# Kernel optimization log

Hardware: AMD Instinct MI355X
Metric: run time of the kernel (lower is better)

The kernel has to match this reference:

```python
import jax, jax.numpy as jnp
import numpy as np

B, C, H, W = 16, 256, 32, 32
NUM_LAYERS = 30
OUT = 16  # sqrt(out_channels)
EPS = 1e-5


def setup_inputs() -> dict:
    key = jax.random.key(0)
    k1, k2, k3 = jax.random.split(key, 3)
    x = jax.random.normal(k1, (B, C, H, W), dtype=jnp.float32)
    # delta_t ~ small positive values (module inits ~N(0.01, 0.005))
    delta_t = jax.random.uniform(k2, (NUM_LAYERS, 1), dtype=jnp.float32) * 0.02
    matrices = jax.random.normal(k3, (NUM_LAYERS, 1, 1, OUT, OUT), dtype=jnp.float32) * 0.1
    gamma = jnp.ones((H * W,), dtype=jnp.float32)   # BatchNorm2d weight, oc = i*i = H*W
    beta = jnp.zeros((H * W,), dtype=jnp.float32)   # BatchNorm2d bias
    return {"x": x, "delta_t": delta_t, "matrices": matrices, "gamma": gamma, "beta": beta}


def _bn_relu6(z, gamma, beta):
    # training-mode BatchNorm2d over channel axis 1 (channels = H*W), then ReLU6
    mean = jnp.mean(z, axis=(0, 2, 3), keepdims=True)
    var = jnp.mean(jnp.square(z - mean), axis=(0, 2, 3), keepdims=True)  # biased var
    zhat = (z - mean) * jax.lax.rsqrt(var + EPS)
    g = gamma.reshape(1, -1, 1, 1)
    b = beta.reshape(1, -1, 1, 1)
    return jnp.clip(zhat * g + b, 0.0, 6.0)


def reference(x, delta_t, matrices, gamma, beta):
    b, c, h, w = x.shape
    hw = h * w
    # feature_reshape: [B,C,H,W] -> [B,HW,C] -> [B,HW,out,out] (inn == out branch)
    x1 = x.reshape(b, c, hw).transpose(0, 2, 1).reshape(b, hw, OUT, OUT)
    dt = jnp.clip(delta_t, 0.0, 6.0)[:, 0]  # relu6(delta_t), shape [L]

    def step(y0, params):
        m, dtl = params  # m: [1,1,out,out] broadcasts elementwise against x1
        dydt = -y0 + _bn_relu6(y0 + m * x1, gamma, beta)
        return y0 + dtl * dydt, None

    y0, _ = jax.lax.scan(step, x1, (matrices, dt))
    # (y0 + x1): [B, HW, out, out] -> view [B,H,W,out*out] -> permute to [B,out*out,H,W]
    y = (y0 + x1).reshape(b, h, w, OUT * OUT).transpose(0, 3, 1, 2)
    return y
```

## Files before the change

### kernel.cpp

```cpp
#include <hip/hip_runtime.h>

typedef float v2f __attribute__((ext_vector_type(2)));
typedef float v4f __attribute__((ext_vector_type(4)));

#define HW      1024
#define NROWS   4096
#define NLAYERS 30
#define TPB     256

static __device__ __forceinline__ v2f pk_fma(v2f a, v2f b, v2f c) {
    v2f d; asm("v_pk_fma_f32 %0, %1, %2, %3" : "=v"(d) : "v"(a), "v"(b), "v"(c));
    return d;
}
static __device__ __forceinline__ v2f pk_add(v2f a, v2f b) {
    v2f d; asm("v_pk_add_f32 %0, %1, %2" : "=v"(d) : "v"(a), "v"(b));
    return d;
}
static __device__ __forceinline__ v2f pk_mul(v2f a, v2f b) {
    v2f d; asm("v_pk_mul_f32 %0, %1, %2" : "=v"(d) : "v"(a), "v"(b));
    return d;
}

template <int CTRL, int RMASK>
__device__ __forceinline__ float dpp_add(float x) {
    int t = __builtin_amdgcn_update_dpp(0, __builtin_bit_cast(int, x),
                                        CTRL, RMASK, 0xf, true);
    return x + __builtin_bit_cast(float, t);
}
__device__ __forceinline__ float wave_sum64(float x) {
    x = dpp_add<0x111, 0xf>(x);
    x = dpp_add<0x112, 0xf>(x);
    x = dpp_add<0x114, 0xf>(x);
    x = dpp_add<0x118, 0xf>(x);
    x = dpp_add<0x142, 0xa>(x);
    x = dpp_add<0x143, 0xc>(x);
    return x;
}
__device__ __forceinline__ float bcast63(float x) {
    return __builtin_bit_cast(float,
        __builtin_amdgcn_readlane(__builtin_bit_cast(int, x), 63));
}

__global__ __launch_bounds__(TPB) void txp64(const float* __restrict__ src,
                                             float* __restrict__ dst,
                                             int M, int N) {
    __shared__ float tile[64][65];
    const int n0 = blockIdx.x * 64;
    const int m0 = blockIdx.y * 64;
    const int tx = threadIdx.x & 63;
    const int ty = threadIdx.x >> 6;
#pragma unroll
    for (int i = 0; i < 16; ++i) {
        const int r = ty + 4 * i;
        tile[r][tx] = src[(size_t)(m0 + r) * N + n0 + tx];
    }
    __syncthreads();
#pragma unroll
    for (int i = 0; i < 16; ++i) {
        const int r = ty + 4 * i;
        dst[(size_t)(n0 + r) * M + m0 + tx] = tile[tx][r];
    }
}

__global__ __launch_bounds__(64, 1) void ode_row1w(
    float* ws, const float* __restrict__ delta_t,
    const float* __restrict__ matrices, const float* __restrict__ gamma,
    const float* __restrict__ beta) {

    const int p    = blockIdx.x;
    const int lane = threadIdx.x;
    float* row = ws + (size_t)p * NROWS;

    v2f x1[32], y[32], z[32];
#pragma unroll
    for (int j = 0; j < 16; ++j) {
        const v4f q4 = *(const v4f*)(row + 4 * lane + 256 * j);
        x1[2 * j]     = (v2f){q4.x, q4.y};
        x1[2 * j + 1] = (v2f){q4.z, q4.w};
        y[2 * j]     = x1[2 * j];
        y[2 * j + 1] = x1[2 * j + 1];
    }

    const float gp = gamma[p];
    const float bp = beta[p];

    v2f sa[4], qa[4];

    {
        const v4f m4 = *(const v4f*)(matrices + 4 * lane);
        const v2f mA = {m4.x, m4.y}, mB = {m4.z, m4.w};
#pragma unroll
        for (int r = 0; r < 4; ++r) { sa[r] = (v2f){0.f, 0.f}; qa[r] = (v2f){0.f, 0.f}; }
#pragma unroll
        for (int j = 0; j < 16; ++j) {
            z[2 * j]     = pk_fma(mA, x1[2 * j], y[2 * j]);
            z[2 * j + 1] = pk_fma(mB, x1[2 * j + 1], y[2 * j + 1]);
            sa[j & 3] = pk_add(sa[j & 3], z[2 * j]);
            qa[j & 3] = pk_fma(z[2 * j], z[2 * j], qa[j & 3]);
            sa[(j + 2) & 3] = pk_add(sa[(j + 2) & 3], z[2 * j + 1]);
            qa[(j + 2) & 3] = pk_fma(z[2 * j + 1], z[2 * j + 1], qa[(j + 2) & 3]);
        }
    }

    v4f   mq  = *(const v4f*)(matrices + 256 + 4 * lane);
    float dtc = delta_t[0];
    float dtn = delta_t[1];

    for (int k = 0; k < NLAYERS - 1; ++k) {
        const int k2 = (k + 2 < NLAYERS) ? k + 2 : NLAYERS - 1;
        const v4f   mq_n  = *(const v4f*)(matrices + k2 * 256 + 4 * lane);
        const float dt_nn = delta_t[k2];

        const v2f sv = pk_add(pk_add(sa[0], sa[1]), pk_add(sa[2], sa[3]));
        const v2f qv = pk_add(pk_add(qa[0], qa[1]), pk_add(qa[2], qa[3]));
        const float S = bcast63(wave_sum64(sv.x + sv.y));
        const float Q = bcast63(wave_sum64(qv.x + qv.y));

        const float dtk  = __builtin_amdgcn_fmed3f(dtc, 0.0f, 6.0f);
        const float mean = S * (1.0f / 4096.0f);
        const float var  = fmaf(-mean, mean, Q * (1.0f / 4096.0f));
        const float rstd = rsqrtf(var + 1e-5f);
        const float g    = gp * rstd;
        const float b    = fmaf(-mean, g, bp);
        const v2f g2 = {g, g}, b2 = {b, b};
        const v2f dt2 = {dtk, dtk};
        const v2f om2 = {1.0f - dtk, 1.0f - dtk};
        const v2f mA = {mq.x, mq.y}, mB = {mq.z, mq.w};

#pragma unroll
        for (int r = 0; r < 4; ++r) { sa[r] = (v2f){0.f, 0.f}; qa[r] = (v2f){0.f, 0.f}; }

#pragma unroll
        for (int j = 0; j < 16; ++j) {
#pragma unroll
            for (int h = 0; h < 2; ++h) {
                const int e = 2 * j + h;
                v2f a = pk_fma(z[e], g2, b2);
                a.x = __builtin_amdgcn_fmed3f(a.x, 0.0f, 6.0f);
                a.y = __builtin_amdgcn_fmed3f(a.y, 0.0f, 6.0f);
                v2f yy = pk_mul(om2, y[e]);
                y[e] = pk_fma(dt2, a, yy);
                z[e] = pk_fma(h ? mB : mA, x1[e], y[e]);
                sa[(j + 2 * h) & 3] = pk_add(sa[(j + 2 * h) & 3], z[e]);
                qa[(j + 2 * h) & 3] = pk_fma(z[e], z[e], qa[(j + 2 * h) & 3]);
            }
        }

        mq = mq_n; dtc = dtn; dtn = dt_nn;
    }

    {
        const v2f sv = pk_add(pk_add(sa[0], sa[1]), pk_add(sa[2], sa[3]));
        const v2f qv = pk_add(pk_add(qa[0], qa[1]), pk_add(qa[2], qa[3]));
        const float S = bcast63(wave_sum64(sv.x + sv.y));
        const float Q = bcast63(wave_sum64(qv.x + qv.y));

        const float dtk  = __builtin_amdgcn_fmed3f(dtc, 0.0f, 6.0f);
        const float mean = S * (1.0f / 4096.0f);
        const float var  = fmaf(-mean, mean, Q * (1.0f / 4096.0f));
        const float rstd = rsqrtf(var + 1e-5f);
        const float g    = gp * rstd;
        const float b    = fmaf(-mean, g, bp);
        const v2f g2 = {g, g}, b2 = {b, b};
        const v2f dt2 = {dtk, dtk};
        const v2f om2 = {1.0f - dtk, 1.0f - dtk};

#pragma unroll
        for (int j = 0; j < 16; ++j) {
            v2f o0, o1;
#pragma unroll
            for (int h = 0; h < 2; ++h) {
                const int e = 2 * j + h;
                v2f a = pk_fma(z[e], g2, b2);
                a.x = __builtin_amdgcn_fmed3f(a.x, 0.0f, 6.0f);
                a.y = __builtin_amdgcn_fmed3f(a.y, 0.0f, 6.0f);
                v2f yy = pk_mul(om2, y[e]);
                yy = pk_fma(dt2, a, yy);
                const v2f o = pk_add(yy, x1[e]);
                if (h == 0) o0 = o; else o1 = o;
            }
            v4f o4; o4.x = o0.x; o4.y = o0.y; o4.z = o1.x; o4.w = o1.y;
            *(v4f*)(row + 4 * lane + 256 * j) = o4;
        }
    }
}

__global__ __launch_bounds__(TPB) void ode_fused(const float* __restrict__ x,
                                                 const float* __restrict__ delta_t,
                                                 const float* __restrict__ matrices,
                                                 const float* __restrict__ gamma,
                                                 const float* __restrict__ beta,
                                                 float* __restrict__ out) {
    const int bid = blockIdx.x;
    const int p   = ((bid & 7) << 7) | (bid >> 3);
    const int t   = threadIdx.x;

    __shared__ float smat[(NLAYERS + 1) * 256];
    __shared__ float sdt[NLAYERS];
    __shared__ __align__(16) v2f red[2][4];

#pragma unroll
    for (int i = 0; i < NLAYERS; ++i)
        smat[i * 256 + t] = matrices[i * 256 + t];
    if (t < NLAYERS)
        sdt[t] = __builtin_amdgcn_fmed3f(delta_t[t], 0.0f, 6.0f);

    v2f x1[8], y[8];
#pragma unroll
    for (int k = 0; k < 8; ++k) {
        x1[k].x = x[(size_t)(t + 512 * k) * HW + p];
        x1[k].y = x[(size_t)(t + 512 * k + 256) * HW + p];
        y[k] = x1[k];
    }

    const float gp   = gamma[p];
    const float bp   = beta[p];
    const int   wid  = t >> 6;
    const int   lane = t & 63;

    __syncthreads();
    float m_cur = smat[t];

    for (int l = 0; l < NLAYERS; ++l) {
        const float dtl = sdt[l];
        const v2f m2    = {m_cur, m_cur};
        const v2f dt2   = {dtl, dtl};
        const v2f om2   = {1.0f - dtl, 1.0f - dtl};

        v2f z[8];
        v2f sA = {0.f, 0.f}, sB = {0.f, 0.f};
        v2f qA = {0.f, 0.f}, qB = {0.f, 0.f};
#pragma unroll
        for (int k = 0; k < 8; k += 2) {
            z[k]     = __builtin_elementwise_fma(m2, x1[k], y[k]);
            z[k + 1] = __builtin_elementwise_fma(m2, x1[k + 1], y[k + 1]);
            sA += z[k];
            sB += z[k + 1];
            qA = __builtin_elementwise_fma(z[k], z[k], qA);
            qB = __builtin_elementwise_fma(z[k + 1], z[k + 1], qB);
        }
#pragma unroll
        for (int k = 0; k < 8; ++k) y[k] *= om2;

        const v2f sv = sA + sB;
        const v2f qv = qA + qB;
        float s = wave_sum64(sv.x + sv.y);
        float q = wave_sum64(qv.x + qv.y);

        const int par = l & 1;
        if (lane == 63) { v2f w; w.x = s; w.y = q; red[par][wid] = w; }
        m_cur = smat[(l + 1) * 256 + t];
        __syncthreads();

        const float4 r0 = *(const float4*)&red[par][0];
        const float4 r1 = *(const float4*)&red[par][2];
        const float S  = (r0.x + r0.z) + (r1.x + r1.z);
        const float S2 = (r0.y + r0.w) + (r1.y + r1.w);

        const float mean = S * (1.0f / 4096.0f);
        const float var  = fmaf(-mean, mean, S2 * (1.0f / 4096.0f));
        const float rstd = rsqrtf(var + 1e-5f);
        const float g    = gp * rstd;
        const float bb   = fmaf(-mean, g, bp);
        const v2f g2 = {g, g}, b2 = {bb, bb};
        const v2f z0 = {0.f, 0.f}, s6 = {6.f, 6.f};
#pragma unroll
        for (int k = 0; k < 8; ++k) {
            v2f a = __builtin_elementwise_fma(z[k], g2, b2);
            a = __builtin_elementwise_max(a, z0);
            a = __builtin_elementwise_min(a, s6);
            y[k] = __builtin_elementwise_fma(dt2, a, y[k]);
        }
    }

#pragma unroll
    for (int k = 0; k < 8; ++k) {
        out[(size_t)(t + 512 * k) * HW + p]       = y[k].x + x1[k].x;
        out[(size_t)(t + 512 * k + 256) * HW + p] = y[k].y + x1[k].y;
    }
}

extern "C" void kernel_launch(void* const* d_in, const int* in_sizes, int n_in,
                              void* d_out, int out_size, void* d_ws, size_t ws_size,
                              hipStream_t stream) {
    const float* x        = (const float*)d_in[0];
    const float* delta_t  = (const float*)d_in[1];
    const float* matrices = (const float*)d_in[2];
    const float* gamma    = (const float*)d_in[3];
    const float* beta     = (const float*)d_in[4];
    float* out = (float*)d_out;

    const size_t need = (size_t)HW * NROWS * sizeof(float);
    if (d_ws != nullptr && ws_size >= need) {
        float* ws = (float*)d_ws;
        txp64<<<dim3(HW / 64, NROWS / 64), dim3(TPB), 0, stream>>>(x, ws, NROWS, HW);
        ode_row1w<<<dim3(HW), dim3(64), 0, stream>>>(ws, delta_t, matrices, gamma, beta);
        txp64<<<dim3(NROWS / 64, HW / 64), dim3(TPB), 0, stream>>>(ws, out, HW, NROWS);
    } else {
        ode_fused<<<dim3(HW), dim3(TPB), 0, stream>>>(x, delta_t, matrices, gamma, beta, out);
    }
}
```

Before: 111.7 us.

## Split each BN channel row across two waves with LDS double-buffered reduction

The per-channel ODE kernel now uses two 64-lane waves per row instead of one, so each lane holds 16 packed pairs instead of 32. Per-layer mean/variance partials are combined through a double-buffered shared-memory slot with one barrier per layer. The aim is to halve per-wave serial work and register pressure, raising wave count and latency hiding across 1024 blocks. In exchange, each of the 30 layers now pays a block barrier and an LDS round trip.

```diff
diff --git a/kernel.cpp b/kernel.cpp
--- a/kernel.cpp
+++ b/kernel.cpp
@@ -36,10 +36,6 @@
     x = dpp_add<0x143, 0xc>(x);
     return x;
 }
-__device__ __forceinline__ float bcast63(float x) {
-    return __builtin_bit_cast(float,
-        __builtin_amdgcn_readlane(__builtin_bit_cast(int, x), 63));
-}
 
 __global__ __launch_bounds__(TPB) void txp64(const float* __restrict__ src,
                                              float* __restrict__ dst,
@@ -62,19 +58,24 @@
     }
 }
 
-__global__ __launch_bounds__(64, 1) void ode_row1w(
+__global__ __launch_bounds__(128, 2) void ode_row2w(
     float* ws, const float* __restrict__ delta_t,
     const float* __restrict__ matrices, const float* __restrict__ gamma,
     const float* __restrict__ beta) {
 
     const int p    = blockIdx.x;
-    const int lane = threadIdx.x;
+    const int t    = threadIdx.x;
+    const int wid  = t >> 6;
+    const int lane = t & 63;
+    const int c0   = (4 * t) & 255;
     float* row = ws + (size_t)p * NROWS;
 
-    v2f x1[32], y[32], z[32];
-#pragma unroll
-    for (int j = 0; j < 16; ++j) {
-        const v4f q4 = *(const v4f*)(row + 4 * lane + 256 * j);
+    __shared__ __align__(16) v2f red[2][2];
+
+    v2f x1[16], y[16], z[16];
+#pragma unroll
+    for (int j = 0; j < 8; ++j) {
+        const v4f q4 = *(const v4f*)(row + 4 * t + 512 * j);
         x1[2 * j]     = (v2f){q4.x, q4.y};
         x1[2 * j + 1] = (v2f){q4.z, q4.w};
         y[2 * j]     = x1[2 * j];
@@ -84,37 +85,40 @@
     const float gp = gamma[p];
     const float bp = beta[p];
 
-    v2f sa[4], qa[4];
-
     {
-        const v4f m4 = *(const v4f*)(matrices + 4 * lane);
+        const v4f m4 = *(const v4f*)(matrices + c0);
         const v2f mA = {m4.x, m4.y}, mB = {m4.z, m4.w};
-#pragma unroll
-        for (int r = 0; r < 4; ++r) { sa[r] = (v2f){0.f, 0.f}; qa[r] = (v2f){0.f, 0.f}; }
-#pragma unroll
-        for (int j = 0; j < 16; ++j) {
+        v2f s0 = {0.f, 0.f}, s1 = {0.f, 0.f}, q0 = {0.f, 0.f}, q1 = {0.f, 0.f};
+#pragma unroll
+        for (int j = 0; j < 8; ++j) {
             z[2 * j]     = pk_fma(mA, x1[2 * j], y[2 * j]);
             z[2 * j + 1] = pk_fma(mB, x1[2 * j + 1], y[2 * j + 1]);
-            sa[j & 3] = pk_add(sa[j & 3], z[2 * j]);
-            qa[j & 3] = pk_fma(z[2 * j], z[2 * j], qa[j & 3]);
-            sa[(j + 2) & 3] = pk_add(sa[(j + 2) & 3], z[2 * j + 1]);
-            qa[(j + 2) & 3] = pk_fma(z[2 * j + 1], z[2 * j + 1], qa[(j + 2) & 3]);
-        }
-    }
-
-    v4f   mq  = *(const v4f*)(matrices + 256 + 4 * lane);
+            s0 = pk_add(s0, z[2 * j]);
+            q0 = pk_fma(z[2 * j], z[2 * j], q0);
+            s1 = pk_add(s1, z[2 * j + 1]);
+            q1 = pk_fma(z[2 * j + 1], z[2 * j + 1], q1);
+        }
+        const v2f sv = pk_add(s0, s1);
+        const v2f qv = pk_add(q0, q1);
+        const float ss = wave_sum64(sv.x + sv.y);
+        const float qq = wave_sum64(qv.x + qv.y);
+        if (lane == 63) red[0][wid] = (v2f){ss, qq};
+    }
+
+    v4f   mq  = *(const v4f*)(matrices + 256 + c0);
     float dtc = delta_t[0];
     float dtn = delta_t[1];
+    __syncthreads();
 
     for (int k = 0; k < NLAYERS - 1; ++k) {
         const int k2 = (k + 2 < NLAYERS) ? k + 2 : NLAYERS - 1;
-        const v4f   mq_n  = *(const v4f*)(matrices + k2 * 256 + 4 * lane);
+        const v4f   mq_n  = *(const v4f*)(matrices + k2 * 256 + c0);
         const float dt_nn = delta_t[k2];
 
-        const v2f sv = pk_add(pk_add(sa[0], sa[1]), pk_add(sa[2], sa[3]));
-        const v2f qv = pk_add(pk_add(qa[0], qa[1]), pk_add(qa[2], qa[3]));
-        const float S = bcast63(wave_sum64(sv.x + sv.y));
-        const float Q = bcast63(wave_sum64(qv.x + qv.y));
+        const int par = k & 1;
+        const v4f r = *(const v4f*)&red[par][0];
+        const float S = r.x + r.z;
+        const float Q = r.y + r.w;
 
         const float dtk  = __builtin_amdgcn_fmed3f(dtc, 0.0f, 6.0f);
         const float mean = S * (1.0f / 4096.0f);
@@ -127,11 +131,9 @@
         const v2f om2 = {1.0f - dtk, 1.0f - dtk};
         const v2f mA = {mq.x, mq.y}, mB = {mq.z, mq.w};
 
-#pragma unroll
-        for (int r = 0; r < 4; ++r) { sa[r] = (v2f){0.f, 0.f}; qa[r] = (v2f){0.f, 0.f}; }
-
-#pragma unroll
-        for (int j = 0; j < 16; ++j) {
+        v2f s0 = {0.f, 0.f}, s1 = {0.f, 0.f}, q0 = {0.f, 0.f}, q1 = {0.f, 0.f};
+#pragma unroll
+        for (int j = 0; j < 8; ++j) {
 #pragma unroll
             for (int h = 0; h < 2; ++h) {
                 const int e = 2 * j + h;
@@ -141,19 +143,24 @@
                 v2f yy = pk_mul(om2, y[e]);
                 y[e] = pk_fma(dt2, a, yy);
                 z[e] = pk_fma(h ? mB : mA, x1[e], y[e]);
-                sa[(j + 2 * h) & 3] = pk_add(sa[(j + 2 * h) & 3], z[e]);
-                qa[(j + 2 * h) & 3] = pk_fma(z[e], z[e], qa[(j + 2 * h) & 3]);
+                if (h == 0) { s0 = pk_add(s0, z[e]); q0 = pk_fma(z[e], z[e], q0); }
+                else        { s1 = pk_add(s1, z[e]); q1 = pk_fma(z[e], z[e], q1); }
             }
         }
+        const v2f sv = pk_add(s0, s1);
+        const v2f qv = pk_add(q0, q1);
+        const float ss = wave_sum64(sv.x + sv.y);
+        const float qq = wave_sum64(qv.x + qv.y);
+        if (lane == 63) red[par ^ 1][wid] = (v2f){ss, qq};
 
         mq = mq_n; dtc = dtn; dtn = dt_nn;
+        __syncthreads();
     }
 
     {
-        const v2f sv = pk_add(pk_add(sa[0], sa[1]), pk_add(sa[2], sa[3]));
-        const v2f qv = pk_add(pk_add(qa[0], qa[1]), pk_add(qa[2], qa[3]));
-        const float S = bcast63(wave_sum64(sv.x + sv.y));
-        const float Q = bcast63(wave_sum64(qv.x + qv.y));
+        const v4f r = *(const v4f*)&red[(NLAYERS - 1) & 1][0];
+        const float S = r.x + r.z;
+        const float Q = r.y + r.w;
 
         const float dtk  = __builtin_amdgcn_fmed3f(dtc, 0.0f, 6.0f);
         const float mean = S * (1.0f / 4096.0f);
@@ -166,7 +173,7 @@
         const v2f om2 = {1.0f - dtk, 1.0f - dtk};
 
 #pragma unroll
-        for (int j = 0; j < 16; ++j) {
+        for (int j = 0; j < 8; ++j) {
             v2f o0, o1;
 #pragma unroll
             for (int h = 0; h < 2; ++h) {
@@ -180,7 +187,7 @@
                 if (h == 0) o0 = o; else o1 = o;
             }
             v4f o4; o4.x = o0.x; o4.y = o0.y; o4.z = o1.x; o4.w = o1.y;
-            *(v4f*)(row + 4 * lane + 256 * j) = o4;
+            *(v4f*)(row + 4 * t + 512 * j) = o4;
         }
     }
 }
@@ -294,7 +301,7 @@
     if (d_ws != nullptr && ws_size >= need) {
         float* ws = (float*)d_ws;
         txp64<<<dim3(HW / 64, NROWS / 64), dim3(TPB), 0, stream>>>(x, ws, NROWS, HW);
-        ode_row1w<<<dim3(HW), dim3(64), 0, stream>>>(ws, delta_t, matrices, gamma, beta);
+        ode_row2w<<<dim3(HW), dim3(128), 0, stream>>>(ws, delta_t, matrices, gamma, beta);
         txp64<<<dim3(NROWS / 64, HW / 64), dim3(TPB), 0, stream>>>(ws, out, HW, NROWS);
     } else {
         ode_fused<<<dim3(HW), dim3(TPB), 0, stream>>>(x, delta_t, matrices, gamma, beta, out);
```

New measurement: 115.3 us. 1.03x slower.

## Track pre-activation z recurrence and keep x1 in LDS to cut registers

Applied to the files above, without the earlier changes.

Rewrites the ODE step to update z = y + m*x1 directly using a combined coefficient (m_next - (1-dt)*m_cur), removing the y register array. The x1 values are stored in shared memory and reloaded each layer instead of living in registers. This reduces VGPR pressure, which may allow more waves per CU, at the cost of LDS reads every layer and shorter reduction accumulator chains.

```diff
diff --git a/kernel.cpp b/kernel.cpp
--- a/kernel.cpp
+++ b/kernel.cpp
@@ -62,57 +62,53 @@
     }
 }
 
-__global__ __launch_bounds__(64, 1) void ode_row1w(
+__global__ __launch_bounds__(64, 1) void ode_zrec(
     float* ws, const float* __restrict__ delta_t,
     const float* __restrict__ matrices, const float* __restrict__ gamma,
     const float* __restrict__ beta) {
 
     const int p    = blockIdx.x;
     const int lane = threadIdx.x;
+    const int c0   = 4 * lane;
     float* row = ws + (size_t)p * NROWS;
 
-    v2f x1[32], y[32], z[32];
-#pragma unroll
-    for (int j = 0; j < 16; ++j) {
-        const v4f q4 = *(const v4f*)(row + 4 * lane + 256 * j);
-        x1[2 * j]     = (v2f){q4.x, q4.y};
-        x1[2 * j + 1] = (v2f){q4.z, q4.w};
-        y[2 * j]     = x1[2 * j];
-        y[2 * j + 1] = x1[2 * j + 1];
-    }
+    __shared__ float xs[NROWS];
 
     const float gp = gamma[p];
     const float bp = beta[p];
 
-    v2f sa[4], qa[4];
+    v2f z[32];
+    v2f s0 = {0.f, 0.f}, s1 = {0.f, 0.f}, q0 = {0.f, 0.f}, q1 = {0.f, 0.f};
 
     {
-        const v4f m4 = *(const v4f*)(matrices + 4 * lane);
+        const v4f m4 = *(const v4f*)(matrices + c0);
         const v2f mA = {m4.x, m4.y}, mB = {m4.z, m4.w};
 #pragma unroll
-        for (int r = 0; r < 4; ++r) { sa[r] = (v2f){0.f, 0.f}; qa[r] = (v2f){0.f, 0.f}; }
-#pragma unroll
         for (int j = 0; j < 16; ++j) {
-            z[2 * j]     = pk_fma(mA, x1[2 * j], y[2 * j]);
-            z[2 * j + 1] = pk_fma(mB, x1[2 * j + 1], y[2 * j + 1]);
-            sa[j & 3] = pk_add(sa[j & 3], z[2 * j]);
-            qa[j & 3] = pk_fma(z[2 * j], z[2 * j], qa[j & 3]);
-            sa[(j + 2) & 3] = pk_add(sa[(j + 2) & 3], z[2 * j + 1]);
-            qa[(j + 2) & 3] = pk_fma(z[2 * j + 1], z[2 * j + 1], qa[(j + 2) & 3]);
-        }
-    }
-
-    v4f   mq  = *(const v4f*)(matrices + 256 + 4 * lane);
+            const v4f x4 = *(const v4f*)(row + 4 * lane + 256 * j);
+            *(v4f*)&xs[4 * lane + 256 * j] = x4;
+            const v2f xA = {x4.x, x4.y}, xB = {x4.z, x4.w};
+            z[2 * j]     = pk_fma(mA, xA, xA);
+            z[2 * j + 1] = pk_fma(mB, xB, xB);
+            s0 = pk_add(s0, z[2 * j]);
+            q0 = pk_fma(z[2 * j], z[2 * j], q0);
+            s1 = pk_add(s1, z[2 * j + 1]);
+            q1 = pk_fma(z[2 * j + 1], z[2 * j + 1], q1);
+        }
+    }
+
+    v4f   mqc = *(const v4f*)(matrices + c0);
+    v4f   mqn = *(const v4f*)(matrices + 256 + c0);
     float dtc = delta_t[0];
     float dtn = delta_t[1];
 
     for (int k = 0; k < NLAYERS - 1; ++k) {
         const int k2 = (k + 2 < NLAYERS) ? k + 2 : NLAYERS - 1;
-        const v4f   mq_n  = *(const v4f*)(matrices + k2 * 256 + 4 * lane);
+        const v4f   mq2   = *(const v4f*)(matrices + k2 * 256 + c0);
         const float dt_nn = delta_t[k2];
 
-        const v2f sv = pk_add(pk_add(sa[0], sa[1]), pk_add(sa[2], sa[3]));
-        const v2f qv = pk_add(pk_add(qa[0], qa[1]), pk_add(qa[2], qa[3]));
+        const v2f sv = pk_add(s0, s1);
+        const v2f qv = pk_add(q0, q1);
         const float S = bcast63(wave_sum64(sv.x + sv.y));
         const float Q = bcast63(wave_sum64(qv.x + qv.y));
 
@@ -122,36 +118,53 @@
         const float rstd = rsqrtf(var + 1e-5f);
         const float g    = gp * rstd;
         const float b    = fmaf(-mean, g, bp);
+        const float om   = 1.0f - dtk;
         const v2f g2 = {g, g}, b2 = {b, b};
         const v2f dt2 = {dtk, dtk};
-        const v2f om2 = {1.0f - dtk, 1.0f - dtk};
-        const v2f mA = {mq.x, mq.y}, mB = {mq.z, mq.w};
-
-#pragma unroll
-        for (int r = 0; r < 4; ++r) { sa[r] = (v2f){0.f, 0.f}; qa[r] = (v2f){0.f, 0.f}; }
+        const v2f om2 = {om, om};
+        const v2f omn = {-om, -om};
+        const v2f mcA = {mqc.x, mqc.y}, mcB = {mqc.z, mqc.w};
+        const v2f mnA = {mqn.x, mqn.y}, mnB = {mqn.z, mqn.w};
+        const v2f dmA = pk_fma(omn, mcA, mnA);
+        const v2f dmB = pk_fma(omn, mcB, mnB);
+
+        s0 = (v2f){0.f, 0.f}; s1 = (v2f){0.f, 0.f};
+        q0 = (v2f){0.f, 0.f}; q1 = (v2f){0.f, 0.f};
 
 #pragma unroll
         for (int j = 0; j < 16; ++j) {
-#pragma unroll
-            for (int h = 0; h < 2; ++h) {
-                const int e = 2 * j + h;
+            const v4f x4 = *(const v4f*)&xs[4 * lane + 256 * j];
+            const v2f xA = {x4.x, x4.y}, xB = {x4.z, x4.w};
+            {
+                const int e = 2 * j;
                 v2f a = pk_fma(z[e], g2, b2);
                 a.x = __builtin_amdgcn_fmed3f(a.x, 0.0f, 6.0f);
                 a.y = __builtin_amdgcn_fmed3f(a.y, 0.0f, 6.0f);
-                v2f yy = pk_mul(om2, y[e]);
-                y[e] = pk_fma(dt2, a, yy);
-                z[e] = pk_fma(h ? mB : mA, x1[e], y[e]);
-                sa[(j + 2 * h) & 3] = pk_add(sa[(j + 2 * h) & 3], z[e]);
-                qa[(j + 2 * h) & 3] = pk_fma(z[e], z[e], qa[(j + 2 * h) & 3]);
+                v2f t = pk_mul(dt2, a);
+                t = pk_fma(dmA, xA, t);
+                z[e] = pk_fma(om2, z[e], t);
+                s0 = pk_add(s0, z[e]);
+                q0 = pk_fma(z[e], z[e], q0);
             }
-        }
-
-        mq = mq_n; dtc = dtn; dtn = dt_nn;
+            {
+                const int e = 2 * j + 1;
+                v2f a = pk_fma(z[e], g2, b2);
+                a.x = __builtin_amdgcn_fmed3f(a.x, 0.0f, 6.0f);
+                a.y = __builtin_amdgcn_fmed3f(a.y, 0.0f, 6.0f);
+                v2f t = pk_mul(dt2, a);
+                t = pk_fma(dmB, xB, t);
+                z[e] = pk_fma(om2, z[e], t);
+                s1 = pk_add(s1, z[e]);
+                q1 = pk_fma(z[e], z[e], q1);
+            }
+        }
+
+        mqc = mqn; mqn = mq2; dtc = dtn; dtn = dt_nn;
     }
 
     {
-        const v2f sv = pk_add(pk_add(sa[0], sa[1]), pk_add(sa[2], sa[3]));
-        const v2f qv = pk_add(pk_add(qa[0], qa[1]), pk_add(qa[2], qa[3]));
+        const v2f sv = pk_add(s0, s1);
+        const v2f qv = pk_add(q0, q1);
         const float S = bcast63(wave_sum64(sv.x + sv.y));
         const float Q = bcast63(wave_sum64(qv.x + qv.y));
 
@@ -161,23 +174,38 @@
         const float rstd = rsqrtf(var + 1e-5f);
         const float g    = gp * rstd;
         const float b    = fmaf(-mean, g, bp);
+        const float om   = 1.0f - dtk;
         const v2f g2 = {g, g}, b2 = {b, b};
         const v2f dt2 = {dtk, dtk};
-        const v2f om2 = {1.0f - dtk, 1.0f - dtk};
+        const v2f om2 = {om, om};
+        const v2f omn = {-om, -om};
+        const v2f one2 = {1.0f, 1.0f};
+        const v2f mcA = {mqc.x, mqc.y}, mcB = {mqc.z, mqc.w};
+        const v2f dmA = pk_fma(omn, mcA, one2);
+        const v2f dmB = pk_fma(omn, mcB, one2);
 
 #pragma unroll
         for (int j = 0; j < 16; ++j) {
+            const v4f x4 = *(const v4f*)&xs[4 * lane + 256 * j];
+            const v2f xA = {x4.x, x4.y}, xB = {x4.z, x4.w};
             v2f o0, o1;
-#pragma unroll
-            for (int h = 0; h < 2; ++h) {
-                const int e = 2 * j + h;
+            {
+                const int e = 2 * j;
                 v2f a = pk_fma(z[e], g2, b2);
                 a.x = __builtin_amdgcn_fmed3f(a.x, 0.0f, 6.0f);
                 a.y = __builtin_amdgcn_fmed3f(a.y, 0.0f, 6.0f);
-                v2f yy = pk_mul(om2, y[e]);
-                yy = pk_fma(dt2, a, yy);
-                const v2f o = pk_add(yy, x1[e]);
-                if (h == 0) o0 = o; else o1 = o;
+                v2f t = pk_mul(dt2, a);
+                t = pk_fma(dmA, xA, t);
+                o0 = pk_fma(om2, z[e], t);
+            }
+            {
+                const int e = 2 * j + 1;
+                v2f a = pk_fma(z[e], g2, b2);
+                a.x = __builtin_amdgcn_fmed3f(a.x, 0.0f, 6.0f);
+                a.y = __builtin_amdgcn_fmed3f(a.y, 0.0f, 6.0f);
+                v2f t = pk_mul(dt2, a);
+                t = pk_fma(dmB, xB, t);
+                o1 = pk_fma(om2, z[e], t);
             }
             v4f o4; o4.x = o0.x; o4.y = o0.y; o4.z = o1.x; o4.w = o1.y;
             *(v4f*)(row + 4 * lane + 256 * j) = o4;
@@ -294,7 +322,7 @@
     if (d_ws != nullptr && ws_size >= need) {
         float* ws = (float*)d_ws;
         txp64<<<dim3(HW / 64, NROWS / 64), dim3(TPB), 0, stream>>>(x, ws, NROWS, HW);
-        ode_row1w<<<dim3(HW), dim3(64), 0, stream>>>(ws, delta_t, matrices, gamma, beta);
+        ode_zrec<<<dim3(HW), dim3(64), 0, stream>>>(ws, delta_t, matrices, gamma, beta);
         txp64<<<dim3(NROWS / 64, HW / 64), dim3(TPB), 0, stream>>>(ws, out, HW, NROWS);
     } else {
         ode_fused<<<dim3(HW), dim3(TPB), 0, stream>>>(x, delta_t, matrices, gamma, beta, out);
```

New measurement: 119.1 us. 6.6% more time.
